# Optimization experiments

Measured on AMD Instinct MI355X. Metric: run time of the kernel, lower is better.

Reference implementation:

```python
import jax, jax.numpy as jnp
import numpy as np

IN_C, HEAD_C, EXPAND_C, OUT_C, TIME_C, H = 512, 64, 2048, 512, 256, 8
EPS = 1e-5

def _layernorm(x, g, b):
    mu = jnp.mean(x, axis=-1, keepdims=True)
    var = jnp.mean((x - mu) ** 2, axis=-1, keepdims=True)
    return (x - mu) * jax.lax.rsqrt(var + EPS) * g + b

def setup_inputs() -> dict:
    key = jax.random.key(0)
    ks = jax.random.split(key, 12)
    B, N = 4, 2048
    qkv_dim = HEAD_C * H * 2 + IN_C * H
    def lin(k, fan_in, fan_out):
        bound = 1.0 / np.sqrt(fan_in)
        kw, kb = jax.random.split(k)
        W = jax.random.uniform(kw, (fan_in, fan_out), jnp.float32, -bound, bound)
        b = jax.random.uniform(kb, (fan_out,), jnp.float32, -bound, bound)
        return W, b
    qkv_w, qkv_b = lin(ks[0], IN_C, qkv_dim)
    merge_w, merge_b = lin(ks[1], IN_C * H, IN_C)
    time_w, time_b = lin(ks[2], TIME_C, TIME_C)
    ff1_w, ff1_b = lin(ks[3], IN_C + TIME_C, EXPAND_C)
    ff2_w, ff2_b = lin(ks[4], EXPAND_C, OUT_C)
    return {
        'x': jax.random.normal(ks[5], (B, N, IN_C), jnp.float32),
        't': jax.random.normal(ks[6], (B, TIME_C), jnp.float32),
        'ln1_g': jnp.ones((IN_C,), jnp.float32), 'ln1_b': jnp.zeros((IN_C,), jnp.float32),
        'qkv_w': qkv_w, 'qkv_b': qkv_b,
        'merge_w': merge_w, 'merge_b': merge_b,
        'time_w': time_w, 'time_b': time_b,
        'ln2_g': jnp.ones((IN_C + TIME_C,), jnp.float32), 'ln2_b': jnp.zeros((IN_C + TIME_C,), jnp.float32),
        'ff1_w': ff1_w, 'ff1_b': ff1_b,
        'ff2_w': ff2_w, 'ff2_b': ff2_b,
    }

def reference(x, t, ln1_g, ln1_b, qkv_w, qkv_b, merge_w, merge_b,
              time_w, time_b, ln2_g, ln2_b, ff1_w, ff1_b, ff2_w, ff2_b):
    B, N, _ = x.shape
    scale = HEAD_C ** -0.5
    qkv = _layernorm(x, ln1_g, ln1_b) @ qkv_w + qkv_b
    q, k, v = jnp.split(qkv, [HEAD_C * H, 2 * HEAD_C * H], axis=-1)
    q = q.reshape(B, N, H, HEAD_C)          # B N H Cq
    k = k.reshape(B, N, H, HEAD_C)
    v = v.reshape(B, N, H, IN_C)            # V per head has dim in_c (as in source)
    attn = jnp.einsum('bnhc,bmhc->bhnm', q, k) * scale
    attn = jax.nn.softmax(attn, axis=-1)    # dropout = identity (eval)
    out = jnp.einsum('bhnm,bmhd->bnhd', attn, v).reshape(B, N, H * IN_C)
    x = x + out @ merge_w + merge_b
    tt = (t @ time_w + time_b)[:, None, :]  # B 1 time_c, broadcasts over N
    tt = jnp.broadcast_to(tt, (B, N, TIME_C))
    h = _layernorm(jnp.concatenate([x, tt], axis=-1), ln2_g, ln2_b)
    h = jax.nn.gelu(h @ ff1_w + ff1_b, approximate=False)
    return x + (h @ ff2_w + ff2_b)          # shortcut = Identity (in_c == out_c)
```

## Files before the change

### kernel.cpp

```cpp
#include <hip/hip_runtime.h>

#define IN_C 512
#define HEAD_C 64
#define NHEAD 8
#define TIME_C 256
#define EXPAND_C 2048
#define NB 4
#define NN 2048
#define QKV_DIM 5120
#define ROWS (NB*NN)
#define MERGE_K (NHEAD*IN_C)
#define LN2_C (IN_C+TIME_C)

typedef __bf16 bf16x8 __attribute__((ext_vector_type(8)));
typedef float f32x4 __attribute__((ext_vector_type(4)));
typedef float f32x16 __attribute__((ext_vector_type(16)));
typedef unsigned int u32x4 __attribute__((ext_vector_type(4)));
typedef unsigned short u16x4v __attribute__((ext_vector_type(4)));

__device__ __forceinline__ unsigned short f2bf(float f){
  unsigned int u = __builtin_bit_cast(unsigned int, f);
  u += 0x7fffu + ((u >> 16) & 1u);
  return (unsigned short)(u >> 16);
}
__device__ __forceinline__ unsigned int cvtpk(float a, float b){
  unsigned int r;
  asm("v_cvt_pk_bf16_f32 %0, %1, %2" : "=v"(r) : "v"(a), "v"(b));
  return r;
}
__device__ __forceinline__ float vexp2(float x){
  float r;
  asm("v_exp_f32 %0, %1" : "=v"(r) : "v"(x));
  return r;
}
__device__ __forceinline__ float bpermf(float v, int srclane){
  int r = __builtin_amdgcn_ds_bpermute(srclane<<2, __builtin_bit_cast(int, v));
  return __builtin_bit_cast(float, r);
}
__device__ __forceinline__ void gload16(const unsigned short* g, unsigned short* l){
  __builtin_amdgcn_global_load_lds(
      (const __attribute__((address_space(1))) void*)g,
      (__attribute__((address_space(3))) void*)l, 16, 0, 0);
}

__global__ __launch_bounds__(256) void k_transpose_w(const float* __restrict__ W,
                                                     unsigned short* __restrict__ Wt,
                                                     int K, int N){
  __shared__ unsigned short tile[64*72];
  int t = threadIdx.x;
  int kb = blockIdx.y<<6, nb = blockIdx.x<<6;
  {
    int kr = t>>2, nc = (t&3)<<4;
    const float* src = W + (size_t)(kb+kr)*N + nb + nc;
    alignas(16) unsigned short tmp[16];
    #pragma unroll
    for (int j=0;j<16;j+=4){
      float4 v = *(const float4*)(src + j);
      tmp[j+0]=f2bf(v.x); tmp[j+1]=f2bf(v.y); tmp[j+2]=f2bf(v.z); tmp[j+3]=f2bf(v.w);
    }
    *(bf16x8*)&tile[kr*72 + nc]     = *(bf16x8*)&tmp[0];
    *(bf16x8*)&tile[kr*72 + nc + 8] = *(bf16x8*)&tmp[8];
  }
  __syncthreads();
  {
    int nr = t>>2, kc = (t&3)<<4;
    alignas(16) unsigned short ov[16];
    #pragma unroll
    for (int i=0;i<16;i++) ov[i] = tile[(kc+i)*72 + nr];
    unsigned short* dst = Wt + (size_t)(nb+nr)*K + kb + kc;
    *(bf16x8*)dst     = *(bf16x8*)&ov[0];
    *(bf16x8*)(dst+8) = *(bf16x8*)&ov[8];
  }
}

__global__ __launch_bounds__(256) void k_repack_k(const unsigned short* __restrict__ qkv,
                                                  unsigned short* __restrict__ Kf){
  __shared__ unsigned short tile[64*72];
  int j = blockIdx.x;
  int kb64 = j&31, bh = j>>5;
  int b = bh>>3, hh = bh&7;
  int t = threadIdx.x;
  {
    int key = t>>2, sc = t&3;
    const unsigned short* src = qkv + (size_t)(b*NN + kb64*64 + key)*QKV_DIM + IN_C + hh*HEAD_C;
    *(bf16x8*)&tile[key*72 + sc*8]     = *(const bf16x8*)(src + sc*8);
    *(bf16x8*)&tile[key*72 + (sc+4)*8] = *(const bf16x8*)(src + (sc+4)*8);
  }
  __syncthreads();
  int l = t&63, w = t>>6;
  int kb32l = w&1, kk0 = w>>1;
  int lkey = l&31;
  int pk = (lkey & ~12) | ((lkey&4)<<1) | ((lkey&8)>>1);
  #pragma unroll
  for (int i=0;i<2;i++){
    int kk = kk0 + i*2;
    alignas(16) unsigned short ov[8];
    #pragma unroll
    for (int jj=0;jj<8;jj++)
      ov[jj] = tile[(kb32l*32 + pk)*72 + kk*16 + (l>>5)*8 + jj];
    size_t dst = (((size_t)(bh*64 + kb64*2 + kb32l))*4 + kk)*512 + l*8;
    *(bf16x8*)(Kf + dst) = *(bf16x8*)ov;
  }
}

__global__ __launch_bounds__(256) void k_repack_v(const unsigned short* __restrict__ qkv,
                                                  unsigned short* __restrict__ Vf){
  __shared__ unsigned short tile[64*136];
  int j = blockIdx.x;
  int kb64 = j&31, bh = j>>5;
  int b = bh>>3, hh = bh&7;
  int t = threadIdx.x, l = t&63, w = t>>6;
  int key = t>>2, sc = t&3;
  const unsigned short* srow = qkv + (size_t)(b*NN + kb64*64 + key)*QKV_DIM + 2*IN_C + hh*IN_C;
  for (int p=0;p<4;p++){
    #pragma unroll
    for (int i=0;i<4;i++){
      int ch = sc + i*4;
      *(bf16x8*)&tile[key*136 + ch*8] = *(const bf16x8*)(srow + p*128 + ch*8);
    }
    __syncthreads();
    #pragma unroll
    for (int dbl=0;dbl<4;dbl++){
      alignas(16) unsigned short ov[8];
      #pragma unroll
      for (int jj=0;jj<8;jj++)
        ov[jj] = tile[(w*16 + (l>>5)*8 + jj)*136 + dbl*32 + (l&31)];
      size_t dst = (((size_t)(bh*128 + kb64*4 + w))*16 + p*4 + dbl)*512 + l*8;
      *(bf16x8*)(Vf + dst) = *(bf16x8*)ov;
    }
    __syncthreads();
  }
}

__global__ __launch_bounds__(256) void k_ln1(const float* __restrict__ x,
                                             const float* __restrict__ g,
                                             const float* __restrict__ bta,
                                             unsigned short* __restrict__ out){
  int row = (blockIdx.x<<2) + (threadIdx.x>>6);
  int l = threadIdx.x&63;
  const float* px = x + (size_t)row*IN_C + l*8;
  alignas(16) float v[8];
  *(float4*)&v[0] = *(const float4*)px;
  *(float4*)&v[4] = *(const float4*)(px+4);
  float s=0.f, sq=0.f;
  #pragma unroll
  for (int j=0;j<8;j++){ s+=v[j]; sq+=v[j]*v[j]; }
  #pragma unroll
  for (int d=32; d>0; d>>=1){ s += __shfl_xor(s,d); sq += __shfl_xor(sq,d); }
  float mu = s*(1.f/IN_C);
  float var = sq*(1.f/IN_C) - mu*mu;
  float rstd = rsqrtf(var + 1e-5f);
  alignas(16) unsigned short o[8];
  #pragma unroll
  for (int j=0;j<8;j++){
    int c = l*8+j;
    o[j] = f2bf((v[j]-mu)*rstd*g[c] + bta[c]);
  }
  *(bf16x8*)(out + (size_t)row*IN_C + l*8) = *(bf16x8*)o;
}

__global__ __launch_bounds__(256) void k_time(const float* __restrict__ t,
                                              const float* __restrict__ W,
                                              const float* __restrict__ bias,
                                              float* __restrict__ tt){
  int b = blockIdx.x, j = threadIdx.x;
  float acc = bias[j];
  const float* tr = t + b*TIME_C;
  #pragma unroll 4
  for (int c=0;c<TIME_C;c++) acc = fmaf(tr[c], W[c*TIME_C + j], acc);
  tt[b*TIME_C + j] = acc;
}

__global__ __launch_bounds__(256) void k_ln2(const float* __restrict__ x2,
                                             const float* __restrict__ tt,
                                             const float* __restrict__ g,
                                             const float* __restrict__ bta,
                                             unsigned short* __restrict__ out){
  int row = (blockIdx.x<<2) + (threadIdx.x>>6);
  int l = threadIdx.x&63;
  int bi = row>>11;
  int c0 = l*12;
  alignas(16) float v[12], gg[12], bb[12];
  #pragma unroll
  for (int q=0;q<3;q++){
    int c = c0 + q*4;
    const float* src = (c < IN_C) ? &x2[(size_t)row*IN_C + c] : &tt[bi*TIME_C + c - IN_C];
    *(float4*)&v[q*4]  = *(const float4*)src;
    *(float4*)&gg[q*4] = *(const float4*)&g[c];
    *(float4*)&bb[q*4] = *(const float4*)&bta[c];
  }
  float s=0.f, sq=0.f;
  #pragma unroll
  for (int j=0;j<12;j++){ s+=v[j]; sq+=v[j]*v[j]; }
  #pragma unroll
  for (int d=32; d>0; d>>=1){ s += __shfl_xor(s,d); sq += __shfl_xor(sq,d); }
  float mu = s*(1.f/LN2_C);
  float var = sq*(1.f/LN2_C) - mu*mu;
  float rstd = rsqrtf(var + 1e-5f);
  alignas(8) unsigned short ov[12];
  #pragma unroll
  for (int j=0;j<12;j++)
    ov[j] = f2bf((v[j]-mu)*rstd*gg[j] + bb[j]);
  unsigned short* po = out + (size_t)row*LN2_C + c0;
  *(u16x4v*)&po[0] = *(u16x4v*)&ov[0];
  *(u16x4v*)&po[4] = *(u16x4v*)&ov[4];
  *(u16x4v*)&po[8] = *(u16x4v*)&ov[8];
}

template<int EPI, int BN>
__global__ __launch_bounds__(256) void k_gemm(const unsigned short* __restrict__ A, int lda,
                                              const unsigned short* __restrict__ Bt, int ldb,
                                              const float* __restrict__ bias,
                                              const float* __restrict__ res, int ldres,
                                              void* __restrict__ Cp, int ldc, int K){
  constexpr int NI = BN/32;
  __shared__ unsigned short sA[128*64];
  __shared__ unsigned short sB[BN*64];
  int t = threadIdx.x;
  int l = t&63, w = t>>6;
  int nxb = gridDim.x;
  int bid = blockIdx.x + nxb*blockIdx.y;
  int cpx = (nxb*gridDim.y) >> 3;
  int sb  = (bid&7)*cpx + (bid>>3);
  int bx  = sb % nxb, by = sb / nxb;
  int m0 = by<<7, n0 = bx*BN;
  int wr = (w>>1)<<6, wc = (w&1)*(BN/2);
  int lm = l&15, kq = (l>>4)<<3;
  f32x4 acc[4][NI] = {};
  int srow = l>>3, scol = (l&7)<<3;
  const unsigned short* pA = A + (size_t)m0*lda;
  const unsigned short* pB = Bt + (size_t)n0*ldb;
  for (int k0=0; k0<K; k0+=64){
    #pragma unroll
    for (int i=0;i<4;i++){
      int c = w*4 + i;
      gload16(pA + (size_t)(c*8 + srow)*lda + k0 + scol, &sA[c*512]);
    }
    #pragma unroll
    for (int i=0;i<BN/32;i++){
      int c = w*(BN/32) + i;
      gload16(pB + (size_t)(c*8 + srow)*ldb + k0 + scol, &sB[c*512]);
    }
    __syncthreads();
    bf16x8 af[2][4], bfv[2][NI];
    #pragma unroll
    for (int kk=0;kk<2;kk++){
      #pragma unroll
      for (int i=0;i<4;i++)
        af[kk][i]  = *(const bf16x8*)&sA[(wr + i*16 + lm)*64 + kk*32 + kq];
      #pragma unroll
      for (int i=0;i<NI;i++)
        bfv[kk][i] = *(const bf16x8*)&sB[(wc + i*16 + lm)*64 + kk*32 + kq];
    }
    #pragma unroll
    for (int kk=0;kk<2;kk++)
      #pragma unroll
      for (int mi=0;mi<4;mi++)
        #pragma unroll
        for (int ni=0;ni<NI;ni++)
          acc[mi][ni] = __builtin_amdgcn_mfma_f32_16x16x32_bf16(af[kk][mi], bfv[kk][ni], acc[mi][ni], 0,0,0);
    __syncthreads();
  }
  int lr4 = (l>>4)<<2;
  #pragma unroll
  for (int mi=0;mi<4;mi++){
    int row0 = m0 + wr + mi*16 + lr4;
    #pragma unroll
    for (int ni=0;ni<NI;ni++){
      int col = n0 + wc + ni*16 + lm;
      float bi = bias[col];
      #pragma unroll
      for (int r=0;r<4;r++){
        float v = acc[mi][ni][r] + bi;
        int row = row0 + r;
        if (EPI==1){
          v += res[(size_t)row*ldres + col];
          ((float*)Cp)[(size_t)row*ldc + col] = v;
        } else if (EPI==2){
          v = 0.5f*v*(1.f + erff(v*0.70710678118f));
          ((unsigned short*)Cp)[(size_t)row*ldc + col] = f2bf(v);
        } else {
          ((unsigned short*)Cp)[(size_t)row*ldc + col] = f2bf(v);
        }
      }
    }
  }
}

__global__ __launch_bounds__(256, 4) void k_attn(const unsigned short* __restrict__ qkv,
                                                 const unsigned short* __restrict__ Kf,
                                                 const unsigned short* __restrict__ Vf,
                                                 unsigned short* __restrict__ out){
  int j = blockIdx.x;
  int xcd = j&7;
  int rest = j>>3;
  int bh = xcd + ((rest>>6)<<3);
  int inner = rest&63;
  int qb = inner>>2, dh = inner&3;
  int b = bh>>3, hh = bh&7;
  int t = threadIdx.x, l = t&63, w = t>>6;
  int q0 = qb*128 + w*32;
  int lq = l&31, half = l>>5;

  bf16x8 qf[4];
  #pragma unroll
  for (int kk=0;kk<4;kk++){
    bf16x8 raw = *(const bf16x8*)(qkv + (size_t)(b*NN + q0 + lq)*QKV_DIM + hh*HEAD_C + kk*16 + half*8);
    u32x4 u = __builtin_bit_cast(u32x4, raw);
    u32x4 rr;
    #pragma unroll
    for (int jj=0;jj<4;jj++){
      float lo = __builtin_bit_cast(float, (u[jj]&0xffffu)<<16);
      float hi = __builtin_bit_cast(float, u[jj]&0xffff0000u);
      rr[jj] = cvtpk(lo*0.18033688f, hi*0.18033688f);
    }
    qf[kk] = __builtin_bit_cast(bf16x8, rr);
  }

  f32x16 o[4] = {};
  float l_ = 0.f;

  const unsigned short* Kbase = Kf + (size_t)bh*64*2048 + l*8;
  const unsigned short* Vbase = Vf + ((size_t)bh*128*16 + dh*4)*512 + l*8;

  for (int c=0;c<64;c++){
    const unsigned short* kp = Kbase + (size_t)c*2048;
    bf16x8 kf0 = *(const bf16x8*)(kp);
    bf16x8 kf1 = *(const bf16x8*)(kp + 512);
    bf16x8 kf2 = *(const bf16x8*)(kp + 1024);
    bf16x8 kf3 = *(const bf16x8*)(kp + 1536);

    f32x16 s = {};
    s = __builtin_amdgcn_mfma_f32_32x32x16_bf16(kf0, qf[0], s, 0,0,0);
    s = __builtin_amdgcn_mfma_f32_32x32x16_bf16(kf1, qf[1], s, 0,0,0);
    s = __builtin_amdgcn_mfma_f32_32x32x16_bf16(kf2, qf[2], s, 0,0,0);
    s = __builtin_amdgcn_mfma_f32_32x32x16_bf16(kf3, qf[3], s, 0,0,0);

    float pv[16]; float ps = 0.f;
    #pragma unroll
    for (int r=0;r<16;r++){
      pv[r] = vexp2(s[r]);
      ps += pv[r];
    }
    l_ += ps;

    bf16x8 pf0 = __builtin_bit_cast(bf16x8, (u32x4){ cvtpk(pv[0],pv[1]),  cvtpk(pv[2],pv[3]),
                                                     cvtpk(pv[4],pv[5]),  cvtpk(pv[6],pv[7]) });
    bf16x8 pf1 = __builtin_bit_cast(bf16x8, (u32x4){ cvtpk(pv[8],pv[9]),  cvtpk(pv[10],pv[11]),
                                                     cvtpk(pv[12],pv[13]),cvtpk(pv[14],pv[15]) });

    const unsigned short* vp = Vbase + (size_t)c*16384;
    {
      bf16x8 v0 = *(const bf16x8*)(vp);
      bf16x8 v1 = *(const bf16x8*)(vp + 512);
      bf16x8 v2 = *(const bf16x8*)(vp + 1024);
      bf16x8 v3 = *(const bf16x8*)(vp + 1536);
      o[0] = __builtin_amdgcn_mfma_f32_32x32x16_bf16(pf0, v0, o[0], 0,0,0);
      o[1] = __builtin_amdgcn_mfma_f32_32x32x16_bf16(pf0, v1, o[1], 0,0,0);
      o[2] = __builtin_amdgcn_mfma_f32_32x32x16_bf16(pf0, v2, o[2], 0,0,0);
      o[3] = __builtin_amdgcn_mfma_f32_32x32x16_bf16(pf0, v3, o[3], 0,0,0);
    }
    {
      bf16x8 v0 = *(const bf16x8*)(vp + 8192);
      bf16x8 v1 = *(const bf16x8*)(vp + 8704);
      bf16x8 v2 = *(const bf16x8*)(vp + 9216);
      bf16x8 v3 = *(const bf16x8*)(vp + 9728);
      o[0] = __builtin_amdgcn_mfma_f32_32x32x16_bf16(pf1, v0, o[0], 0,0,0);
      o[1] = __builtin_amdgcn_mfma_f32_32x32x16_bf16(pf1, v1, o[1], 0,0,0);
      o[2] = __builtin_amdgcn_mfma_f32_32x32x16_bf16(pf1, v2, o[2], 0,0,0);
      o[3] = __builtin_amdgcn_mfma_f32_32x32x16_bf16(pf1, v3, o[3], 0,0,0);
    }
  }

  l_ += __shfl_xor(l_, 32);
  float invl = 1.f / l_;
  #pragma unroll
  for (int r=0;r<16;r++){
    int qr = (r&3) + 8*(r>>2) + 4*half;
    float il = bpermf(invl, qr);
    size_t row = (size_t)(b*NN + q0 + qr);
    #pragma unroll
    for (int dn=0;dn<4;dn++){
      int col = hh*IN_C + dh*128 + dn*32 + lq;
      out[row*MERGE_K + col] = f2bf(o[dn][r]*il);
    }
  }
}

extern "C" void kernel_launch(void* const* d_in, const int* in_sizes, int n_in,
                              void* d_out, int out_size, void* d_ws, size_t ws_size,
                              hipStream_t stream){
  const float* x       = (const float*)d_in[0];
  const float* tin     = (const float*)d_in[1];
  const float* ln1_g   = (const float*)d_in[2];
  const float* ln1_b   = (const float*)d_in[3];
  const float* qkv_w   = (const float*)d_in[4];
  const float* qkv_b   = (const float*)d_in[5];
  const float* merge_w = (const float*)d_in[6];
  const float* merge_b = (const float*)d_in[7];
  const float* time_w  = (const float*)d_in[8];
  const float* time_b  = (const float*)d_in[9];
  const float* ln2_g   = (const float*)d_in[10];
  const float* ln2_b   = (const float*)d_in[11];
  const float* ff1_w   = (const float*)d_in[12];
  const float* ff1_b   = (const float*)d_in[13];
  const float* ff2_w   = (const float*)d_in[14];
  const float* ff2_b   = (const float*)d_in[15];

  char* ws = (char*)d_ws;
  size_t off = 0;
  auto alloc = [&](size_t bytes)->void*{ void* p = ws + off; off += (bytes + 255) & ~(size_t)255; return p; };
  unsigned short* wqkvT   = (unsigned short*)alloc((size_t)QKV_DIM*IN_C*2);
  unsigned short* wmergeT = (unsigned short*)alloc((size_t)IN_C*MERGE_K*2);
  unsigned short* wff1T   = (unsigned short*)alloc((size_t)EXPAND_C*LN2_C*2);
  unsigned short* wff2T   = (unsigned short*)alloc((size_t)IN_C*EXPAND_C*2);
  float*          ttb     = (float*)alloc((size_t)NB*TIME_C*4);
  unsigned short* ln1o    = (unsigned short*)alloc((size_t)ROWS*IN_C*2);
  unsigned short* qkvb    = (unsigned short*)alloc((size_t)ROWS*QKV_DIM*2);
  unsigned short* kfrag   = (unsigned short*)alloc((size_t)32*64*4*64*8*2);
  unsigned short* vfrag   = (unsigned short*)alloc((size_t)32*128*16*64*8*2);
  unsigned short* atto    = (unsigned short*)alloc((size_t)ROWS*MERGE_K*2);
  float*          x2      = (float*)alloc((size_t)ROWS*IN_C*4);
  unsigned short* ln2o = vfrag;
  unsigned short* hbuf = qkvb;

  k_transpose_w<<<dim3(QKV_DIM/64, IN_C/64),  256, 0, stream>>>(qkv_w,   wqkvT,   IN_C,     QKV_DIM);
  k_transpose_w<<<dim3(IN_C/64,   MERGE_K/64),256, 0, stream>>>(merge_w, wmergeT, MERGE_K,  IN_C);
  k_transpose_w<<<dim3(EXPAND_C/64, LN2_C/64),256, 0, stream>>>(ff1_w,   wff1T,   LN2_C,    EXPAND_C);
  k_transpose_w<<<dim3(IN_C/64,   EXPAND_C/64),256, 0, stream>>>(ff2_w,  wff2T,   EXPAND_C, IN_C);
  k_time<<<dim3(NB), 256, 0, stream>>>(tin, time_w, time_b, ttb);
  k_ln1<<<dim3(ROWS/4), 256, 0, stream>>>(x, ln1_g, ln1_b, ln1o);

  k_gemm<0,128><<<dim3(QKV_DIM/128, ROWS/128), 256, 0, stream>>>(ln1o, IN_C, wqkvT, IN_C, qkv_b, nullptr, 0, qkvb, QKV_DIM, IN_C);
  k_repack_k<<<dim3(1024), 256, 0, stream>>>(qkvb, kfrag);
  k_repack_v<<<dim3(1024), 256, 0, stream>>>(qkvb, vfrag);
  k_attn<<<dim3(2048), 256, 0, stream>>>(qkvb, kfrag, vfrag, atto);
  k_gemm<1,64><<<dim3(IN_C/64, ROWS/128), 256, 0, stream>>>(atto, MERGE_K, wmergeT, MERGE_K, merge_b, x, IN_C, x2, IN_C, MERGE_K);
  k_ln2<<<dim3(ROWS/4), 256, 0, stream>>>(x2, ttb, ln2_g, ln2_b, ln2o);
  k_gemm<2,128><<<dim3(EXPAND_C/128, ROWS/128), 256, 0, stream>>>(ln2o, LN2_C, wff1T, LN2_C, ff1_b, nullptr, 0, hbuf, EXPAND_C, LN2_C);
  k_gemm<1,64><<<dim3(IN_C/64, ROWS/128), 256, 0, stream>>>(hbuf, EXPAND_C, wff2T, EXPAND_C, ff2_b, x2, IN_C, (float*)d_out, IN_C, EXPAND_C);

  (void)in_sizes; (void)n_in; (void)out_size; (void)ws_size;
}
```

Baseline: 587.2 us.

## Switch attention to 16x16x32 MFMA tiles with wider head-dim split

Moves the attention kernel from 32x32x16 to 16x16x32 bf16 MFMA. Each wave now handles 16 queries over a 256-wide slice of the value dimension, instead of 32 queries over 128. The K and V repack kernels and fragment buffers are relaid out to match the new operand formats. This halves the redundant QK^T and exp work repeated across value-dimension splits. In exchange, each wave issues more V fragment loads and K is reused across fewer queries, which raises load traffic per query.

```diff
diff --git a/kernel.cpp b/kernel.cpp
--- a/kernel.cpp
+++ b/kernel.cpp
@@ -14,7 +14,6 @@
 
 typedef __bf16 bf16x8 __attribute__((ext_vector_type(8)));
 typedef float f32x4 __attribute__((ext_vector_type(4)));
-typedef float f32x16 __attribute__((ext_vector_type(16)));
 typedef unsigned int u32x4 __attribute__((ext_vector_type(4)));
 typedef unsigned short u16x4v __attribute__((ext_vector_type(4)));
 
@@ -88,17 +87,19 @@
   }
   __syncthreads();
   int l = t&63, w = t>>6;
-  int kb32l = w&1, kk0 = w>>1;
-  int lkey = l&31;
-  int pk = (lkey & ~12) | ((lkey&4)<<1) | ((lkey&8)>>1);
+  int kcl = w>>1;
+  int p = l&15;
+  int hdj = (l>>4)*8;
   #pragma unroll
   for (int i=0;i<2;i++){
-    int kk = kk0 + i*2;
+    int gh = (w&1)*2 + i;
+    int g = gh>>1, h = gh&1;
+    int key = kcl*32 + ((p>>2)*8 + g*4 + (p&3));
     alignas(16) unsigned short ov[8];
     #pragma unroll
     for (int jj=0;jj<8;jj++)
-      ov[jj] = tile[(kb32l*32 + pk)*72 + kk*16 + (l>>5)*8 + jj];
-    size_t dst = (((size_t)(bh*64 + kb64*2 + kb32l))*4 + kk)*512 + l*8;
+      ov[jj] = tile[key*72 + h*32 + hdj + jj];
+    size_t dst = (((size_t)(bh*64 + kb64*2 + kcl))*4 + gh)*512 + l*8;
     *(bf16x8*)(Kf + dst) = *(bf16x8*)ov;
   }
 }
@@ -120,12 +121,15 @@
     }
     __syncthreads();
     #pragma unroll
-    for (int dbl=0;dbl<4;dbl++){
+    for (int i=0;i<4;i++){
+      int f = w*4 + i;
+      int kcl = f>>3, dt8 = f&7;
+      int dt = p*8 + dt8;
       alignas(16) unsigned short ov[8];
       #pragma unroll
       for (int jj=0;jj<8;jj++)
-        ov[jj] = tile[(w*16 + (l>>5)*8 + jj)*136 + dbl*32 + (l&31)];
-      size_t dst = (((size_t)(bh*128 + kb64*4 + w))*16 + p*4 + dbl)*512 + l*8;
+        ov[jj] = tile[(kcl*32 + (l>>4)*8 + jj)*136 + dt8*16 + (l&15)];
+      size_t dst = (((size_t)(bh*64 + kb64*2 + kcl))*32 + dt)*512 + l*8;
       *(bf16x8*)(Vf + dst) = *(bf16x8*)ov;
     }
     __syncthreads();
@@ -296,16 +300,16 @@
   int rest = j>>3;
   int bh = xcd + ((rest>>6)<<3);
   int inner = rest&63;
-  int qb = inner>>2, dh = inner&3;
+  int qs = inner>>1, dh = inner&1;
   int b = bh>>3, hh = bh&7;
   int t = threadIdx.x, l = t&63, w = t>>6;
-  int q0 = qb*128 + w*32;
-  int lq = l&31, half = l>>5;
-
-  bf16x8 qf[4];
-  #pragma unroll
-  for (int kk=0;kk<4;kk++){
-    bf16x8 raw = *(const bf16x8*)(qkv + (size_t)(b*NN + q0 + lq)*QKV_DIM + hh*HEAD_C + kk*16 + half*8);
+  int q0 = qs*64 + w*16;
+  int lp = l&15, lg = l>>4;
+
+  bf16x8 qf[2];
+  #pragma unroll
+  for (int kk=0;kk<2;kk++){
+    bf16x8 raw = *(const bf16x8*)(qkv + (size_t)(b*NN + q0 + lp)*QKV_DIM + hh*HEAD_C + kk*32 + lg*8);
     u32x4 u = __builtin_bit_cast(u32x4, raw);
     u32x4 rr;
     #pragma unroll
@@ -317,72 +321,61 @@
     qf[kk] = __builtin_bit_cast(bf16x8, rr);
   }
 
-  f32x16 o[4] = {};
+  f32x4 o[16];
+  #pragma unroll
+  for (int i=0;i<16;i++) o[i] = (f32x4){0.f,0.f,0.f,0.f};
   float l_ = 0.f;
 
-  const unsigned short* Kbase = Kf + (size_t)bh*64*2048 + l*8;
-  const unsigned short* Vbase = Vf + ((size_t)bh*128*16 + dh*4)*512 + l*8;
+  const unsigned short* Kbase = Kf + (size_t)bh*64*4*512 + l*8;
+  const unsigned short* Vbase = Vf + ((size_t)bh*64*32 + dh*16)*512 + l*8;
 
   for (int c=0;c<64;c++){
-    const unsigned short* kp = Kbase + (size_t)c*2048;
+    const unsigned short* kp = Kbase + (size_t)c*4*512;
     bf16x8 kf0 = *(const bf16x8*)(kp);
     bf16x8 kf1 = *(const bf16x8*)(kp + 512);
     bf16x8 kf2 = *(const bf16x8*)(kp + 1024);
     bf16x8 kf3 = *(const bf16x8*)(kp + 1536);
 
-    f32x16 s = {};
-    s = __builtin_amdgcn_mfma_f32_32x32x16_bf16(kf0, qf[0], s, 0,0,0);
-    s = __builtin_amdgcn_mfma_f32_32x32x16_bf16(kf1, qf[1], s, 0,0,0);
-    s = __builtin_amdgcn_mfma_f32_32x32x16_bf16(kf2, qf[2], s, 0,0,0);
-    s = __builtin_amdgcn_mfma_f32_32x32x16_bf16(kf3, qf[3], s, 0,0,0);
-
-    float pv[16]; float ps = 0.f;
-    #pragma unroll
-    for (int r=0;r<16;r++){
-      pv[r] = vexp2(s[r]);
-      ps += pv[r];
-    }
-    l_ += ps;
-
-    bf16x8 pf0 = __builtin_bit_cast(bf16x8, (u32x4){ cvtpk(pv[0],pv[1]),  cvtpk(pv[2],pv[3]),
-                                                     cvtpk(pv[4],pv[5]),  cvtpk(pv[6],pv[7]) });
-    bf16x8 pf1 = __builtin_bit_cast(bf16x8, (u32x4){ cvtpk(pv[8],pv[9]),  cvtpk(pv[10],pv[11]),
-                                                     cvtpk(pv[12],pv[13]),cvtpk(pv[14],pv[15]) });
-
-    const unsigned short* vp = Vbase + (size_t)c*16384;
-    {
-      bf16x8 v0 = *(const bf16x8*)(vp);
-      bf16x8 v1 = *(const bf16x8*)(vp + 512);
-      bf16x8 v2 = *(const bf16x8*)(vp + 1024);
-      bf16x8 v3 = *(const bf16x8*)(vp + 1536);
-      o[0] = __builtin_amdgcn_mfma_f32_32x32x16_bf16(pf0, v0, o[0], 0,0,0);
-      o[1] = __builtin_amdgcn_mfma_f32_32x32x16_bf16(pf0, v1, o[1], 0,0,0);
-      o[2] = __builtin_amdgcn_mfma_f32_32x32x16_bf16(pf0, v2, o[2], 0,0,0);
-      o[3] = __builtin_amdgcn_mfma_f32_32x32x16_bf16(pf0, v3, o[3], 0,0,0);
-    }
-    {
-      bf16x8 v0 = *(const bf16x8*)(vp + 8192);
-      bf16x8 v1 = *(const bf16x8*)(vp + 8704);
-      bf16x8 v2 = *(const bf16x8*)(vp + 9216);
-      bf16x8 v3 = *(const bf16x8*)(vp + 9728);
-      o[0] = __builtin_amdgcn_mfma_f32_32x32x16_bf16(pf1, v0, o[0], 0,0,0);
-      o[1] = __builtin_amdgcn_mfma_f32_32x32x16_bf16(pf1, v1, o[1], 0,0,0);
-      o[2] = __builtin_amdgcn_mfma_f32_32x32x16_bf16(pf1, v2, o[2], 0,0,0);
-      o[3] = __builtin_amdgcn_mfma_f32_32x32x16_bf16(pf1, v3, o[3], 0,0,0);
-    }
-  }
-
+    f32x4 s1 = {0.f,0.f,0.f,0.f}, s2 = {0.f,0.f,0.f,0.f};
+    s1 = __builtin_amdgcn_mfma_f32_16x16x32_bf16(kf0, qf[0], s1, 0,0,0);
+    s1 = __builtin_amdgcn_mfma_f32_16x16x32_bf16(kf1, qf[1], s1, 0,0,0);
+    s2 = __builtin_amdgcn_mfma_f32_16x16x32_bf16(kf2, qf[0], s2, 0,0,0);
+    s2 = __builtin_amdgcn_mfma_f32_16x16x32_bf16(kf3, qf[1], s2, 0,0,0);
+
+    float pv[8];
+    pv[0]=vexp2(s1[0]); pv[1]=vexp2(s1[1]); pv[2]=vexp2(s1[2]); pv[3]=vexp2(s1[3]);
+    pv[4]=vexp2(s2[0]); pv[5]=vexp2(s2[1]); pv[6]=vexp2(s2[2]); pv[7]=vexp2(s2[3]);
+    l_ += ((pv[0]+pv[1])+(pv[2]+pv[3])) + ((pv[4]+pv[5])+(pv[6]+pv[7]));
+
+    bf16x8 pf = __builtin_bit_cast(bf16x8, (u32x4){ cvtpk(pv[0],pv[1]), cvtpk(pv[2],pv[3]),
+                                                    cvtpk(pv[4],pv[5]), cvtpk(pv[6],pv[7]) });
+
+    const unsigned short* vp = Vbase + (size_t)c*32*512;
+    #pragma unroll
+    for (int dq=0;dq<4;dq++){
+      bf16x8 v0 = *(const bf16x8*)(vp + (dq*4+0)*512);
+      bf16x8 v1 = *(const bf16x8*)(vp + (dq*4+1)*512);
+      bf16x8 v2 = *(const bf16x8*)(vp + (dq*4+2)*512);
+      bf16x8 v3 = *(const bf16x8*)(vp + (dq*4+3)*512);
+      o[dq*4+0] = __builtin_amdgcn_mfma_f32_16x16x32_bf16(pf, v0, o[dq*4+0], 0,0,0);
+      o[dq*4+1] = __builtin_amdgcn_mfma_f32_16x16x32_bf16(pf, v1, o[dq*4+1], 0,0,0);
+      o[dq*4+2] = __builtin_amdgcn_mfma_f32_16x16x32_bf16(pf, v2, o[dq*4+2], 0,0,0);
+      o[dq*4+3] = __builtin_amdgcn_mfma_f32_16x16x32_bf16(pf, v3, o[dq*4+3], 0,0,0);
+    }
+  }
+
+  l_ += __shfl_xor(l_, 16);
   l_ += __shfl_xor(l_, 32);
   float invl = 1.f / l_;
   #pragma unroll
-  for (int r=0;r<16;r++){
-    int qr = (r&3) + 8*(r>>2) + 4*half;
+  for (int r=0;r<4;r++){
+    int qr = lg*4 + r;
     float il = bpermf(invl, qr);
     size_t row = (size_t)(b*NN + q0 + qr);
     #pragma unroll
-    for (int dn=0;dn<4;dn++){
-      int col = hh*IN_C + dh*128 + dn*32 + lq;
-      out[row*MERGE_K + col] = f2bf(o[dn][r]*il);
+    for (int dt=0;dt<16;dt++){
+      int col = hh*IN_C + dh*256 + dt*16 + lp;
+      out[row*MERGE_K + col] = f2bf(o[dt][r]*il);
     }
   }
 }
@@ -417,8 +410,8 @@
   float*          ttb     = (float*)alloc((size_t)NB*TIME_C*4);
   unsigned short* ln1o    = (unsigned short*)alloc((size_t)ROWS*IN_C*2);
   unsigned short* qkvb    = (unsigned short*)alloc((size_t)ROWS*QKV_DIM*2);
-  unsigned short* kfrag   = (unsigned short*)alloc((size_t)32*64*4*64*8*2);
-  unsigned short* vfrag   = (unsigned short*)alloc((size_t)32*128*16*64*8*2);
+  unsigned short* kfrag   = (unsigned short*)alloc((size_t)32*64*4*512*2);
+  unsigned short* vfrag   = (unsigned short*)alloc((size_t)32*64*32*512*2);
   unsigned short* atto    = (unsigned short*)alloc((size_t)ROWS*MERGE_K*2);
   float*          x2      = (float*)alloc((size_t)ROWS*IN_C*4);
   unsigned short* ln2o = vfrag;
```

Result: slower. 651.2 us (+10.9%).
